# Performance work log

Measured on AMD Instinct MI355X. Metric: run time of the kernel, lower is better.

Reference implementation:

```python
import jax, jax.numpy as jnp
import numpy as np

B, T, C = 4, 2048, 1024
H, D = 16, 64           # num_heads, head_size
R = D // 2              # rotary_ndims = 32


def _make_rope(T, R):
    # RotaryEmbedding(dim=R): inv_freq over arange(0, R, 2)
    inv_freq = 1.0 / (10000.0 ** (np.arange(0, R, 2, dtype=np.float32) / R))
    t = np.arange(T, dtype=np.float32)
    freqs = np.einsum('i,j->ij', t, inv_freq)        # [T, R/2]
    emb = np.concatenate([freqs, freqs], axis=-1)    # [T, R]
    return jnp.asarray(np.stack([np.cos(emb), np.sin(emb)]), dtype=jnp.float32)  # [2, T, R]


def setup_inputs() -> dict:
    key = jax.random.key(0)
    ks = jax.random.split(key, 10)
    s = 1.0 / np.sqrt(C)
    inp = {
        'x': jax.random.normal(ks[0], (B, T, C), dtype=jnp.float32),
        'RoPE': _make_rope(T, R),
        'key_padding_mask': jax.random.randint(ks[1], (B, T), 0, 2, dtype=jnp.int32),
        'Wq': jax.random.normal(ks[2], (C, C), dtype=jnp.float32) * s,
        'bq': jnp.zeros((C,), dtype=jnp.float32),
        'Wk': jax.random.normal(ks[3], (C, C), dtype=jnp.float32) * s,
        'bk': jnp.zeros((C,), dtype=jnp.float32),
        'Wv': jax.random.normal(ks[4], (C, C), dtype=jnp.float32) * s,
        'bv': jnp.zeros((C,), dtype=jnp.float32),
        'Wo': jax.random.normal(ks[5], (C, C), dtype=jnp.float32) * s,
        'bo': jnp.zeros((C,), dtype=jnp.float32),
    }
    return inp


def _rotate_half(x):
    x1, x2 = x[..., : x.shape[-1] // 2], x[..., x.shape[-1] // 2:]
    return jnp.concatenate([-x2, x1], axis=-1)


def reference(x, RoPE, key_padding_mask, Wq, bq, Wk, bk, Wv, bv, Wo, bo):
    Bx, Tx, Cx = x.shape
    # projections -> [B, H, T, D]
    def proj(W, b):
        return (x @ W.T + b).reshape(Bx, Tx, H, D).transpose(0, 2, 1, 3)
    q, k, v = proj(Wq, bq), proj(Wk, bk), proj(Wv, bv)

    # partial rotary: first R dims rotated, rest passed through
    q_rot, q_pass = q[..., :R], q[..., R:]
    k_rot, k_pass = k[..., :R], k[..., R:]
    cos, sin = RoPE[0][:Tx], RoPE[1][:Tx]            # [T, R]
    q_rot = q_rot * cos + _rotate_half(q_rot) * sin
    k_rot = k_rot * cos + _rotate_half(k_rot) * sin
    q = jnp.concatenate([q_rot, q_pass], axis=-1)
    k = jnp.concatenate([k_rot, k_pass], axis=-1)

    att = jnp.einsum('bhqd,bhkd->bhqk', q, k) * (1.0 / np.sqrt(D))
    mask = key_padding_mask[:, None, None, :]        # [B,1,1,T]
    att = jnp.where(mask == 0, jnp.asarray(-1e30, att.dtype), att)
    att = jax.nn.softmax(att, axis=-1)
    out = jnp.einsum('bhqk,bhkd->bhqd', att, v)      # [B,H,T,D]
    out = out.transpose(0, 2, 1, 3).reshape(Bx, Tx, Cx)
    return out @ Wo.T + bo
```

## Files before the change

kernel.cpp:

```cpp
#include <hip/hip_runtime.h>
#include <stdint.h>


typedef __attribute__((ext_vector_type(8))) short bf16x8;
typedef __attribute__((ext_vector_type(4))) float f32x4;
typedef __attribute__((ext_vector_type(4))) short short4v;
typedef __attribute__((ext_vector_type(2))) uint32_t uint2v;

#define MFMA16(a, b, c) __builtin_amdgcn_mfma_f32_16x16x32_bf16((a), (b), (c), 0, 0, 0)

#if __has_builtin(__builtin_amdgcn_exp2f)
#define FEXP(x) __builtin_amdgcn_exp2f(x)
#define QSCALE 0.18033688011112042f
#else
#define FEXP(x) __expf(x)
#define QSCALE 0.125f
#endif

static __device__ __forceinline__ short f2bf(float f) {
  union { float fv; uint32_t u; } v; v.fv = f;
  uint32_t r = v.u + 0x7FFFu + ((v.u >> 16) & 1u);
  return (short)(r >> 16);
}

static __device__ __forceinline__ uint32_t pack_trunc(float a, float b) {
  union { float f; uint32_t u; } ua, ub;
  ua.f = a; ub.f = b;
#if __has_builtin(__builtin_amdgcn_perm)
  return __builtin_amdgcn_perm(ub.u, ua.u, 0x07060302u);
#else
  return (ub.u & 0xFFFF0000u) | (ua.u >> 16);
#endif
}

typedef __attribute__((address_space(1))) void as1_void;
typedef __attribute__((address_space(3))) void as3_void;
static __device__ __forceinline__ void gld_lds16(const void* g, void* l) {
  __builtin_amdgcn_global_load_lds((as1_void*)g, (as3_void*)l, 16, 0, 0);
}

__global__ __launch_bounds__(256) void cvt_kernel(
    const float* x, const float* wq, const float* wk, const float* wv,
    const float* wo,
    short* xb, short* wqb, short* wkb, short* wvb, short* wob) {
  int64_t g = (int64_t)blockIdx.x * 256 + threadIdx.x;
  const int64_t NX = 8388608 / 4, NW = 1048576 / 4;
  const float* src;
  short* dst;
  int64_t i;
  if (g < NX)               { src = x;  dst = xb;  i = g; }
  else if (g < NX + NW)     { src = wq; dst = wqb; i = g - NX; }
  else if (g < NX + 2 * NW) { src = wk; dst = wkb; i = g - NX - NW; }
  else if (g < NX + 3 * NW) { src = wv; dst = wvb; i = g - NX - 2 * NW; }
  else                      { src = wo; dst = wob; i = g - NX - 3 * NW; }
  float4 v = ((const float4*)src)[i];
  short4v o;
  o[0] = f2bf(v.x); o[1] = f2bf(v.y); o[2] = f2bf(v.z); o[3] = f2bf(v.w);
  *(short4v*)&dst[i * 4] = o;
}

__global__ __launch_bounds__(256, 2) void qkv3_gemm(
    const short* __restrict__ Xb,
    const short* __restrict__ Wq, const short* __restrict__ Wk,
    const short* __restrict__ Wv,
    const float* __restrict__ bq, const float* __restrict__ bk,
    const float* __restrict__ bv,
    const float* __restrict__ rope, const int* __restrict__ mask,
    short* __restrict__ Qh, short* __restrict__ Kh, short* __restrict__ Vt) {
  __shared__ __align__(16) short As[2][128 * 32];
  __shared__ __align__(16) short Bs[2][3][128 * 32];

  const int t = threadIdx.x;
  const int lane = t & 63;
  const int wave = t >> 6;
  const int c = lane & 15;
  const int quad = lane >> 4;
  const int m0 = blockIdx.x * 128;
  const int n0 = blockIdx.y * 128;

  f32x4 zero4 = {0.f, 0.f, 0.f, 0.f};
  f32x4 acc[3][4][4];
#pragma unroll
  for (int m = 0; m < 3; ++m)
#pragma unroll
    for (int i = 0; i < 4; ++i)
#pragma unroll
      for (int j = 0; j < 4; ++j) acc[m][i][j] = zero4;

  const int wm = wave & 1, wn = wave >> 1;

  const int srow = t >> 2;
  const int gc = ((t & 3) - (srow >> 2)) & 3;
  const short* gA = Xb + (size_t)(m0 + srow) * 1024 + gc * 8;
  const short* gW0 = Wq + (size_t)(n0 + srow) * 1024 + gc * 8;
  const short* gW1 = Wk + (size_t)(n0 + srow) * 1024 + gc * 8;
  const short* gW2 = Wv + (size_t)(n0 + srow) * 1024 + gc * 8;

#define QKV_STAGE(buf, k0)                                  \
  do {                                                      \
    gld_lds16(gA + (k0), &As[buf][t * 8]);                  \
    gld_lds16(gA + (k0) + 65536, &As[buf][t * 8 + 2048]);   \
    gld_lds16(gW0 + (k0), &Bs[buf][0][t * 8]);              \
    gld_lds16(gW0 + (k0) + 65536, &Bs[buf][0][t * 8 + 2048]); \
    gld_lds16(gW1 + (k0), &Bs[buf][1][t * 8]);              \
    gld_lds16(gW1 + (k0) + 65536, &Bs[buf][1][t * 8 + 2048]); \
    gld_lds16(gW2 + (k0), &Bs[buf][2][t * 8]);              \
    gld_lds16(gW2 + (k0) + 65536, &Bs[buf][2][t * 8 + 2048]); \
  } while (0)

  QKV_STAGE(0, 0);

  for (int ki = 0; ki < 32; ++ki) {
    __syncthreads();
    if (ki < 31) QKV_STAGE((ki + 1) & 1, (ki + 1) * 32);

    const short* as = &As[ki & 1][0];
    bf16x8 af[4];
#pragma unroll
    for (int i = 0; i < 4; ++i) {
      int mr = wm * 64 + i * 16 + c;
      af[i] = *(const bf16x8*)&as[mr * 32 + (((quad + (mr >> 2)) & 3) * 8)];
    }
#pragma unroll
    for (int m = 0; m < 3; ++m) {
      const short* bs = &Bs[ki & 1][m][0];
      bf16x8 bfr[4];
#pragma unroll
      for (int j = 0; j < 4; ++j) {
        int nr = wn * 64 + j * 16 + c;
        bfr[j] = *(const bf16x8*)&bs[nr * 32 + (((quad + (nr >> 2)) & 3) * 8)];
      }
#pragma unroll
      for (int i = 0; i < 4; ++i)
#pragma unroll
        for (int j = 0; j < 4; ++j)
          acc[m][i][j] = MFMA16(af[i], bfr[j], acc[m][i][j]);
    }
  }
#undef QKV_STAGE

  const int nb = n0 + wn * 64;
  const int hcol = nb >> 6;
  const int bidx = m0 >> 11;
  const int tbase = (m0 & 2047) + wm * 64 + quad * 4;
  const int* mrow = mask + bidx * 2048;

#pragma unroll
  for (int mat = 0; mat < 2; ++mat) {
    short* Og = (mat == 0) ? Qh : Kh;
    const float* bias = (mat == 0) ? bq : bk;
    float bj[4];
#pragma unroll
    for (int j = 0; j < 4; ++j) bj[j] = bias[nb + j * 16 + c];
    size_t hb = (size_t)(bidx * 16 + hcol) * 2048;
#pragma unroll
    for (int i = 0; i < 4; ++i) {
#pragma unroll
      for (int r = 0; r < 4; ++r) {
        int tp = tbase + i * 16 + r;
        float f = (mat == 0) ? QSCALE : (mrow[tp] ? 1.0f : 0.0f);
        float cosv = rope[tp * 32 + c];
        float sinv = rope[65536 + tp * 32 + c];
        float v0 = acc[mat][i][0][r] + bj[0];
        float v1 = acc[mat][i][1][r] + bj[1];
        float v2 = acc[mat][i][2][r] + bj[2];
        float v3 = acc[mat][i][3][r] + bj[3];
        size_t base = (hb + tp) * 64;
        Og[base + c]      = f2bf((v0 * cosv - v1 * sinv) * f);
        Og[base + 16 + c] = f2bf((v1 * cosv + v0 * sinv) * f);
        Og[base + 32 + c] = f2bf(v2 * f);
        Og[base + 48 + c] = f2bf(v3 * f);
      }
    }
  }
  {
    float bj[4];
#pragma unroll
    for (int j = 0; j < 4; ++j) bj[j] = bv[nb + j * 16 + c];
    size_t hb = (size_t)(bidx * 16 + hcol) * 64;
#pragma unroll
    for (int i = 0; i < 4; ++i) {
      int tp = tbase + i * 16;
      int4 mv = *(const int4*)&mrow[tp];
      float fr[4];
      fr[0] = mv.x ? 1.f : 0.f; fr[1] = mv.y ? 1.f : 0.f;
      fr[2] = mv.z ? 1.f : 0.f; fr[3] = mv.w ? 1.f : 0.f;
#pragma unroll
      for (int j = 0; j < 4; ++j) {
        short4v pv;
#pragma unroll
        for (int r = 0; r < 4; ++r)
          pv[r] = f2bf((acc[2][i][j][r] + bj[j]) * fr[r]);
        size_t base = (hb + j * 16 + c) * 2048 + tp;
        *(short4v*)&Vt[base] = pv;
      }
    }
  }
}

__global__ __launch_bounds__(256, 2) void attn_kernel(
    const short* __restrict__ Qh, const short* __restrict__ Kh,
    const short* __restrict__ Vt, const int* __restrict__ mask,
    short* __restrict__ Og) {
  __shared__ __align__(16) short Ks[2][64 * 64];
  __shared__ __align__(16) short Vs[2][64 * 64];
  __shared__ __align__(16) short Pl[4][32 * 64];
  __shared__ float nmw[4];

  const int t = threadIdx.x;
  const int lane = t & 63;
  const int wave = t >> 6;
  const int c = lane & 15;
  const int quad = lane >> 4;
  const int qt = blockIdx.x;
  const int bh = blockIdx.y;
  const int bidx = bh >> 4;
  const short* Qg = Qh + ((size_t)bh * 2048 + qt * 256) * 64;
  const short* Kg = Kh + (size_t)bh * 2048 * 64;
  const short* Vg = Vt + (size_t)bh * 64 * 2048;

  {
    const int4* mr = (const int4*)(mask + bidx * 2048);
    int4 a = mr[t * 2], b = mr[t * 2 + 1];
    int cnt = (a.x == 0) + (a.y == 0) + (a.z == 0) + (a.w == 0) +
              (b.x == 0) + (b.y == 0) + (b.z == 0) + (b.w == 0);
    cnt += __shfl_xor(cnt, 1);  cnt += __shfl_xor(cnt, 2);
    cnt += __shfl_xor(cnt, 4);  cnt += __shfl_xor(cnt, 8);
    cnt += __shfl_xor(cnt, 16); cnt += __shfl_xor(cnt, 32);
    if (lane == 0) nmw[wave] = (float)cnt;
  }

  bf16x8 qf[2][4];
#pragma unroll
  for (int ks = 0; ks < 2; ++ks)
#pragma unroll
    for (int it = 0; it < 4; ++it)
      qf[ks][it] =
          *(const bf16x8*)&Qg[(wave * 64 + it * 16 + c) * 64 + ks * 32 + quad * 8];

  const bf16x8 ones = {0x3F80, 0x3F80, 0x3F80, 0x3F80,
                       0x3F80, 0x3F80, 0x3F80, 0x3F80};

  f32x4 zero4 = {0.f, 0.f, 0.f, 0.f};
  f32x4 O[4][4];
#pragma unroll
  for (int dt = 0; dt < 4; ++dt)
#pragma unroll
    for (int it = 0; it < 4; ++it) O[dt][it] = zero4;
  f32x4 Ol[4] = {zero4, zero4, zero4, zero4};

  const int krow0 = t >> 3;
  const int klc = (t & 7) ^ (krow0 & 7);
  const short* gk0 = Kg + (size_t)krow0 * 64 + klc * 8;
  const short* gv0 = Vg + (size_t)krow0 * 2048 + klc * 8;
  short* Pw = &Pl[wave][0];

  gld_lds16(gk0, &Ks[0][t * 8]);
  gld_lds16(gk0 + 32 * 64, &Ks[0][t * 8 + 2048]);
  gld_lds16(gv0, &Vs[0][t * 8]);
  gld_lds16(gv0 + 32 * 2048, &Vs[0][t * 8 + 2048]);

  for (int ci = 0; ci < 32; ++ci) {
    __syncthreads();
    if (ci < 31) {
      int cn = (ci + 1) * 64;
      int nb = (ci + 1) & 1;
      gld_lds16(gk0 + (size_t)cn * 64, &Ks[nb][t * 8]);
      gld_lds16(gk0 + (size_t)(cn + 32) * 64, &Ks[nb][t * 8 + 2048]);
      gld_lds16(gv0 + cn, &Vs[nb][t * 8]);
      gld_lds16(gv0 + cn + 32 * 2048, &Vs[nb][t * 8 + 2048]);
    }
    const short* ksb = &Ks[ci & 1][0];
    const short* vsb = &Vs[ci & 1][0];

    bf16x8 ak[2][4], av[2][4];
#pragma unroll
    for (int ks = 0; ks < 2; ++ks)
#pragma unroll
      for (int jt = 0; jt < 4; ++jt) {
        ak[ks][jt] = *(const bf16x8*)&ksb[(jt * 16 + c) * 64 +
                                          (((4 * ks + quad) ^ (c & 7)) * 8)];
        av[ks][jt] = *(const bf16x8*)&vsb[(jt * 16 + c) * 64 +
                                          (((4 * ks + quad) ^ (c & 7)) * 8)];
      }

#pragma unroll
    for (int h = 0; h < 2; ++h) {
      f32x4 St[4][2];
#pragma unroll
      for (int jt = 0; jt < 4; ++jt) {
        St[jt][0] = MFMA16(ak[0][jt], qf[0][h * 2 + 0], zero4);
        St[jt][1] = MFMA16(ak[0][jt], qf[0][h * 2 + 1], zero4);
      }
#pragma unroll
      for (int jt = 0; jt < 4; ++jt) {
        St[jt][0] = MFMA16(ak[1][jt], qf[1][h * 2 + 0], St[jt][0]);
        St[jt][1] = MFMA16(ak[1][jt], qf[1][h * 2 + 1], St[jt][1]);
      }

#pragma unroll
      for (int itl = 0; itl < 2; ++itl) {
#pragma unroll
        for (int jt = 0; jt < 4; ++jt) {
          float p0 = FEXP(St[jt][itl][0]);
          float p1 = FEXP(St[jt][itl][1]);
          float p2 = FEXP(St[jt][itl][2]);
          float p3 = FEXP(St[jt][itl][3]);
          uint2v pk;
          pk[0] = pack_trunc(p0, p1);
          pk[1] = pack_trunc(p2, p3);
          *(uint2v*)&Pw[(itl * 16 + c) * 64 +
                        (((jt * 2 + (quad >> 1)) ^ (c & 7)) * 8) +
                        (quad & 1) * 4] = pk;
        }
      }
      asm volatile("s_waitcnt lgkmcnt(0)" ::: "memory");

#pragma unroll
      for (int ks = 0; ks < 2; ++ks) {
        bf16x8 bp0 =
            *(const bf16x8*)&Pw[c * 64 + (((ks * 4 + quad) ^ (c & 7)) * 8)];
        bf16x8 bp1 =
            *(const bf16x8*)&Pw[(16 + c) * 64 + (((ks * 4 + quad) ^ (c & 7)) * 8)];
        Ol[h * 2 + 0] = MFMA16(ones, bp0, Ol[h * 2 + 0]);
        Ol[h * 2 + 1] = MFMA16(ones, bp1, Ol[h * 2 + 1]);
#pragma unroll
        for (int dt = 0; dt < 4; ++dt) {
          O[dt][h * 2 + 0] = MFMA16(av[ks][dt], bp0, O[dt][h * 2 + 0]);
          O[dt][h * 2 + 1] = MFMA16(av[ks][dt], bp1, O[dt][h * 2 + 1]);
        }
      }
    }
  }

  float nm = nmw[0] + nmw[1] + nmw[2] + nmw[3];
#pragma unroll
  for (int it = 0; it < 4; ++it) {
    float inv = 1.0f / (Ol[it][0] - nm);
    int tq = qt * 256 + wave * 64 + it * 16 + c;
    size_t rb = ((size_t)bidx * 2048 + tq) * 1024 + (size_t)(bh & 15) * 64;
#pragma unroll
    for (int dt = 0; dt < 4; ++dt) {
      short4v ov;
#pragma unroll
      for (int r = 0; r < 4; ++r) ov[r] = f2bf(O[dt][it][r] * inv);
      *(short4v*)&Og[rb + dt * 16 + quad * 4] = ov;
    }
  }
}

__global__ __launch_bounds__(256) void out_gemm(
    const short* __restrict__ Ab, const short* __restrict__ Wob,
    const float* __restrict__ bo, float* __restrict__ out) {
  __shared__ __align__(16) short As[2][64 * 32];
  __shared__ __align__(16) short Bs[2][128 * 32];

  const int t = threadIdx.x;
  const int lane = t & 63;
  const int wave = t >> 6;
  const int c = lane & 15;
  const int quad = lane >> 4;
  const int m0 = blockIdx.x * 64;
  const int n0 = blockIdx.y * 128;

  f32x4 zero4 = {0.f, 0.f, 0.f, 0.f};
  f32x4 acc[4][2];
#pragma unroll
  for (int i = 0; i < 4; ++i) {
    acc[i][0] = zero4;
    acc[i][1] = zero4;
  }

  const int srow = t >> 2;
  const int gc = ((t & 3) - (srow >> 2)) & 3;
  const short* gA = Ab + (size_t)(m0 + srow) * 1024 + gc * 8;
  const short* gB = Wob + (size_t)(n0 + srow) * 1024 + gc * 8;

#define OUT_STAGE(buf, k0)                                   \
  do {                                                       \
    gld_lds16(gA + (k0), &As[buf][t * 8]);                   \
    gld_lds16(gB + (k0), &Bs[buf][t * 8]);                   \
    gld_lds16(gB + (k0) + 65536, &Bs[buf][t * 8 + 2048]);    \
  } while (0)

  OUT_STAGE(0, 0);

  for (int ki = 0; ki < 32; ++ki) {
    __syncthreads();
    if (ki < 31) OUT_STAGE((ki + 1) & 1, (ki + 1) * 32);

    const short* as = &As[ki & 1][0];
    const short* bs = &Bs[ki & 1][0];
    bf16x8 af[4], bfr[2];
#pragma unroll
    for (int i = 0; i < 4; ++i) {
      int mr = i * 16 + c;
      af[i] = *(const bf16x8*)&as[mr * 32 + (((quad + (mr >> 2)) & 3) * 8)];
    }
#pragma unroll
    for (int j = 0; j < 2; ++j) {
      int nr = wave * 32 + j * 16 + c;
      bfr[j] = *(const bf16x8*)&bs[nr * 32 + (((quad + (nr >> 2)) & 3) * 8)];
    }
#pragma unroll
    for (int i = 0; i < 4; ++i) {
      acc[i][0] = MFMA16(af[i], bfr[0], acc[i][0]);
      acc[i][1] = MFMA16(af[i], bfr[1], acc[i][1]);
    }
  }
#undef OUT_STAGE

  const int nb = n0 + wave * 32;
  float bj[2];
  bj[0] = bo[nb + c];
  bj[1] = bo[nb + 16 + c];
#pragma unroll
  for (int i = 0; i < 4; ++i) {
    int m = m0 + i * 16 + quad * 4;
#pragma unroll
    for (int r = 0; r < 4; ++r) {
      float* orow = out + (size_t)(m + r) * 1024 + nb;
      orow[c]      = acc[i][0][r] + bj[0];
      orow[16 + c] = acc[i][1][r] + bj[1];
    }
  }
}

extern "C" void kernel_launch(void* const* d_in, const int* in_sizes, int n_in,
                              void* d_out, int out_size, void* d_ws,
                              size_t ws_size, hipStream_t stream) {
  const float* x    = (const float*)d_in[0];
  const float* rope = (const float*)d_in[1];
  const int*   mask = (const int*)d_in[2];
  const float* Wq   = (const float*)d_in[3];
  const float* bq   = (const float*)d_in[4];
  const float* Wk   = (const float*)d_in[5];
  const float* bk   = (const float*)d_in[6];
  const float* Wv   = (const float*)d_in[7];
  const float* bv   = (const float*)d_in[8];
  const float* Wo   = (const float*)d_in[9];
  const float* bo   = (const float*)d_in[10];
  float* out = (float*)d_out;

  char* ws = (char*)d_ws;
  short* xb  = (short*)(ws);
  short* wqb = (short*)(ws + 16777216);
  short* wkb = (short*)(ws + 18874368);
  short* wvb = (short*)(ws + 20971520);
  short* wob = (short*)(ws + 23068672);
  short* Qh  = (short*)(ws + 25198592);
  short* Kh  = (short*)(ws + 41975808);
  short* Vt  = (short*)(ws + 58753024);
  short* att = xb;

  cvt_kernel<<<12288, 256, 0, stream>>>(x, Wq, Wk, Wv, Wo, xb, wqb, wkb, wvb,
                                        wob);
  qkv3_gemm<<<dim3(64, 8), 256, 0, stream>>>(xb, wqb, wkb, wvb, bq, bk, bv,
                                             rope, mask, Qh, Kh, Vt);
  attn_kernel<<<dim3(8, 64), 256, 0, stream>>>(Qh, Kh, Vt, mask, att);
  out_gemm<<<dim3(128, 8), 256, 0, stream>>>(att, wob, bo, out);
}
```

Measured before the change: 272.9 us.

## Halve attention query tile per block to raise occupancy and grid size

The attention kernel now processes 128 queries per block (32 per wave) instead of 256, doubling the grid to 1024 blocks and cutting per-wave accumulator registers and the P staging buffer in LDS. Launch bounds request 4 blocks per CU instead of 2. The grid is reordered so the head index is the fast dimension. Each wave now counts masked keys itself, removing the shared-memory reduction. The cost is that each block re-streams the full K/V sequence for half as many queries, doubling K/V load traffic and reducing MFMA reuse of each loaded K/V fragment.

Result: no change. 275.9 us (+1.1%).

```diff
diff --git a/kernel.cpp b/kernel.cpp
--- a/kernel.cpp
+++ b/kernel.cpp
@@ -198,56 +198,59 @@
   }
 }
 
-__global__ __launch_bounds__(256, 2) void attn_kernel(
+__global__ __launch_bounds__(256, 4) void attn_kernel(
     const short* __restrict__ Qh, const short* __restrict__ Kh,
     const short* __restrict__ Vt, const int* __restrict__ mask,
     short* __restrict__ Og) {
   __shared__ __align__(16) short Ks[2][64 * 64];
   __shared__ __align__(16) short Vs[2][64 * 64];
-  __shared__ __align__(16) short Pl[4][32 * 64];
-  __shared__ float nmw[4];
+  __shared__ __align__(16) short Pl[4][16 * 64];
 
   const int t = threadIdx.x;
   const int lane = t & 63;
   const int wave = t >> 6;
   const int c = lane & 15;
   const int quad = lane >> 4;
-  const int qt = blockIdx.x;
-  const int bh = blockIdx.y;
+  const int bh = blockIdx.x;
+  const int qt = blockIdx.y;
   const int bidx = bh >> 4;
-  const short* Qg = Qh + ((size_t)bh * 2048 + qt * 256) * 64;
+  const short* Qg = Qh + ((size_t)bh * 2048 + qt * 128) * 64;
   const short* Kg = Kh + (size_t)bh * 2048 * 64;
   const short* Vg = Vt + (size_t)bh * 64 * 2048;
 
+  float nm;
   {
     const int4* mr = (const int4*)(mask + bidx * 2048);
-    int4 a = mr[t * 2], b = mr[t * 2 + 1];
-    int cnt = (a.x == 0) + (a.y == 0) + (a.z == 0) + (a.w == 0) +
-              (b.x == 0) + (b.y == 0) + (b.z == 0) + (b.w == 0);
+    int cnt = 0;
+#pragma unroll
+    for (int k = 0; k < 8; ++k) {
+      int4 a = mr[k * 64 + lane];
+      cnt += (a.x == 0) + (a.y == 0) + (a.z == 0) + (a.w == 0);
+    }
     cnt += __shfl_xor(cnt, 1);  cnt += __shfl_xor(cnt, 2);
     cnt += __shfl_xor(cnt, 4);  cnt += __shfl_xor(cnt, 8);
     cnt += __shfl_xor(cnt, 16); cnt += __shfl_xor(cnt, 32);
-    if (lane == 0) nmw[wave] = (float)cnt;
-  }
-
-  bf16x8 qf[2][4];
+    nm = (float)cnt;
+  }
+
+  bf16x8 qf[2][2];
 #pragma unroll
   for (int ks = 0; ks < 2; ++ks)
 #pragma unroll
-    for (int it = 0; it < 4; ++it)
+    for (int it = 0; it < 2; ++it)
       qf[ks][it] =
-          *(const bf16x8*)&Qg[(wave * 64 + it * 16 + c) * 64 + ks * 32 + quad * 8];
+          *(const bf16x8*)&Qg[(wave * 32 + it * 16 + c) * 64 + ks * 32 + quad * 8];
 
   const bf16x8 ones = {0x3F80, 0x3F80, 0x3F80, 0x3F80,
                        0x3F80, 0x3F80, 0x3F80, 0x3F80};
 
   f32x4 zero4 = {0.f, 0.f, 0.f, 0.f};
-  f32x4 O[4][4];
+  f32x4 O[4][2];
 #pragma unroll
   for (int dt = 0; dt < 4; ++dt)
 #pragma unroll
-    for (int it = 0; it < 4; ++it) O[dt][it] = zero4;
-  f32x4 Ol[4] = {zero4, zero4, zero4, zero4};
+    for (int it = 0; it < 2; ++it) O[dt][it] = zero4;
+  f32x4 Ol[2] = {zero4, zero4};
 
   const int krow0 = t >> 3;
   const int klc = (t & 7) ^ (krow0 & 7);
@@ -285,59 +288,46 @@
       }
 
 #pragma unroll
-    for (int h = 0; h < 2; ++h) {
-      f32x4 St[4][2];
+    for (int it = 0; it < 2; ++it) {
+      f32x4 St[4];
+#pragma unroll
+      for (int jt = 0; jt < 4; ++jt)
+        St[jt] = MFMA16(ak[0][jt], qf[0][it], zero4);
+#pragma unroll
+      for (int jt = 0; jt < 4; ++jt)
+        St[jt] = MFMA16(ak[1][jt], qf[1][it], St[jt]);
+
 #pragma unroll
       for (int jt = 0; jt < 4; ++jt) {
-        St[jt][0] = MFMA16(ak[0][jt], qf[0][h * 2 + 0], zero4);
-        St[jt][1] = MFMA16(ak[0][jt], qf[0][h * 2 + 1], zero4);
-      }
-#pragma unroll
-      for (int jt = 0; jt < 4; ++jt) {
-        St[jt][0] = MFMA16(ak[1][jt], qf[1][h * 2 + 0], St[jt][0]);
-        St[jt][1] = MFMA16(ak[1][jt], qf[1][h * 2 + 1], St[jt][1]);
-      }
-
-#pragma unroll
-      for (int itl = 0; itl < 2; ++itl) {
-#pragma unroll
-        for (int jt = 0; jt < 4; ++jt) {
-          float p0 = FEXP(St[jt][itl][0]);
-          float p1 = FEXP(St[jt][itl][1]);
-          float p2 = FEXP(St[jt][itl][2]);
-          float p3 = FEXP(St[jt][itl][3]);
-          uint2v pk;
-          pk[0] = pack_trunc(p0, p1);
-          pk[1] = pack_trunc(p2, p3);
-          *(uint2v*)&Pw[(itl * 16 + c) * 64 +
-                        (((jt * 2 + (quad >> 1)) ^ (c & 7)) * 8) +
-                        (quad & 1) * 4] = pk;
-        }
+        float p0 = FEXP(St[jt][0]);
+        float p1 = FEXP(St[jt][1]);
+        float p2 = FEXP(St[jt][2]);
+        float p3 = FEXP(St[jt][3]);
+        uint2v pk;
+        pk[0] = pack_trunc(p0, p1);
+        pk[1] = pack_trunc(p2, p3);
+        *(uint2v*)&Pw[c * 64 +
+                      (((jt * 2 + (quad >> 1)) ^ (c & 7)) * 8) +
+                      (quad & 1) * 4] = pk;
       }
       asm volatile("s_waitcnt lgkmcnt(0)" ::: "memory");
 
 #pragma unroll
       for (int ks = 0; ks < 2; ++ks) {
-        bf16x8 bp0 =
+        bf16x8 bp =
             *(const bf16x8*)&Pw[c * 64 + (((ks * 4 + quad) ^ (c & 7)) * 8)];
-        bf16x8 bp1 =
-            *(const bf16x8*)&Pw[(16 + c) * 64 + (((ks * 4 + quad) ^ (c & 7)) * 8)];
-        Ol[h * 2 + 0] = MFMA16(ones, bp0, Ol[h * 2 + 0]);
-        Ol[h * 2 + 1] = MFMA16(ones, bp1, Ol[h * 2 + 1]);
-#pragma unroll
-        for (int dt = 0; dt < 4; ++dt) {
-          O[dt][h * 2 + 0] = MFMA16(av[ks][dt], bp0, O[dt][h * 2 + 0]);
-          O[dt][h * 2 + 1] = MFMA16(av[ks][dt], bp1, O[dt][h * 2 + 1]);
-        }
-      }
-    }
-  }
-
-  float nm = nmw[0] + nmw[1] + nmw[2] + nmw[3];
-#pragma unroll
-  for (int it = 0; it < 4; ++it) {
+        Ol[it] = MFMA16(ones, bp, Ol[it]);
+#pragma unroll
+        for (int dt = 0; dt < 4; ++dt)
+          O[dt][it] = MFMA16(av[ks][dt], bp, O[dt][it]);
+      }
+    }
+  }
+
+#pragma unroll
+  for (int it = 0; it < 2; ++it) {
     float inv = 1.0f / (Ol[it][0] - nm);
-    int tq = qt * 256 + wave * 64 + it * 16 + c;
+    int tq = qt * 128 + wave * 32 + it * 16 + c;
     size_t rb = ((size_t)bidx * 2048 + tq) * 1024 + (size_t)(bh & 15) * 64;
 #pragma unroll
     for (int dt = 0; dt < 4; ++dt) {
@@ -457,6 +447,6 @@
                                         wob);
   qkv3_gemm<<<dim3(64, 8), 256, 0, stream>>>(xb, wqb, wkb, wvb, bq, bk, bv,
                                              rope, mask, Qh, Kh, Vt);
-  attn_kernel<<<dim3(8, 64), 256, 0, stream>>>(Qh, Kh, Vt, mask, att);
+  attn_kernel<<<dim3(64, 16), 256, 0, stream>>>(Qh, Kh, Vt, mask, att);
   out_gemm<<<dim3(128, 8), 256, 0, stream>>>(att, wob, bo, out);
 }
```

## Double-buffer per-wave P tiles, relax LDS waits, reorder attention grid

Applied to the files above, without the earlier changes.

Each wave's P scratch in the attention kernel now has two halves, one per h-iteration. All exp/pack writes for both halves are issued before the PV MFMAs, and partial lgkmcnt waits replace the full drain so LDS writes overlap with compute. The masked-key count is now computed redundantly per wave, removing the shared nmw array and its implicit cross-wave dependency. The grid is transposed so blocks sharing a batch-head are launched adjacently, which may improve K/V cache reuse. LDS use grows by 16KB per block, which may reduce occupancy. The hand-counted lgkmcnt values are fragile and must match the compiler's instruction ordering.

Measured after the change: 266.4 us. 1.02x faster.

```diff
diff --git a/kernel.cpp b/kernel.cpp
--- a/kernel.cpp
+++ b/kernel.cpp
@@ -204,30 +204,33 @@
     short* __restrict__ Og) {
   __shared__ __align__(16) short Ks[2][64 * 64];
   __shared__ __align__(16) short Vs[2][64 * 64];
-  __shared__ __align__(16) short Pl[4][32 * 64];
-  __shared__ float nmw[4];
+  __shared__ __align__(16) short Pl[4][2][32 * 64];
 
   const int t = threadIdx.x;
   const int lane = t & 63;
   const int wave = t >> 6;
   const int c = lane & 15;
   const int quad = lane >> 4;
-  const int qt = blockIdx.x;
-  const int bh = blockIdx.y;
+  const int bh = blockIdx.x;
+  const int qt = blockIdx.y;
   const int bidx = bh >> 4;
   const short* Qg = Qh + ((size_t)bh * 2048 + qt * 256) * 64;
   const short* Kg = Kh + (size_t)bh * 2048 * 64;
   const short* Vg = Vt + (size_t)bh * 64 * 2048;
 
+  float nm;
   {
     const int4* mr = (const int4*)(mask + bidx * 2048);
-    int4 a = mr[t * 2], b = mr[t * 2 + 1];
-    int cnt = (a.x == 0) + (a.y == 0) + (a.z == 0) + (a.w == 0) +
-              (b.x == 0) + (b.y == 0) + (b.z == 0) + (b.w == 0);
+    int cnt = 0;
+#pragma unroll
+    for (int k = 0; k < 8; ++k) {
+      int4 a = mr[k * 64 + lane];
+      cnt += (a.x == 0) + (a.y == 0) + (a.z == 0) + (a.w == 0);
+    }
     cnt += __shfl_xor(cnt, 1);  cnt += __shfl_xor(cnt, 2);
     cnt += __shfl_xor(cnt, 4);  cnt += __shfl_xor(cnt, 8);
     cnt += __shfl_xor(cnt, 16); cnt += __shfl_xor(cnt, 32);
-    if (lane == 0) nmw[wave] = (float)cnt;
+    nm = (float)cnt;
   }
 
   bf16x8 qf[2][4];
@@ -253,7 +256,6 @@
   const int klc = (t & 7) ^ (krow0 & 7);
   const short* gk0 = Kg + (size_t)krow0 * 64 + klc * 8;
   const short* gv0 = Vg + (size_t)krow0 * 2048 + klc * 8;
-  short* Pw = &Pl[wave][0];
 
   gld_lds16(gk0, &Ks[0][t * 8]);
   gld_lds16(gk0 + 32 * 64, &Ks[0][t * 8 + 2048]);
@@ -297,7 +299,7 @@
         St[jt][0] = MFMA16(ak[1][jt], qf[1][h * 2 + 0], St[jt][0]);
         St[jt][1] = MFMA16(ak[1][jt], qf[1][h * 2 + 1], St[jt][1]);
       }
-
+      short* Ph = &Pl[wave][h][0];
 #pragma unroll
       for (int itl = 0; itl < 2; ++itl) {
 #pragma unroll
@@ -309,19 +311,25 @@
           uint2v pk;
           pk[0] = pack_trunc(p0, p1);
           pk[1] = pack_trunc(p2, p3);
-          *(uint2v*)&Pw[(itl * 16 + c) * 64 +
+          *(uint2v*)&Ph[(itl * 16 + c) * 64 +
                         (((jt * 2 + (quad >> 1)) ^ (c & 7)) * 8) +
                         (quad & 1) * 4] = pk;
         }
       }
-      asm volatile("s_waitcnt lgkmcnt(0)" ::: "memory");
-
+      asm volatile("" ::: "memory");
+    }
+
+    asm volatile("s_waitcnt lgkmcnt(8)" ::: "memory");
+
+#pragma unroll
+    for (int h = 0; h < 2; ++h) {
+      const short* Ph = &Pl[wave][h][0];
 #pragma unroll
       for (int ks = 0; ks < 2; ++ks) {
         bf16x8 bp0 =
-            *(const bf16x8*)&Pw[c * 64 + (((ks * 4 + quad) ^ (c & 7)) * 8)];
+            *(const bf16x8*)&Ph[c * 64 + (((ks * 4 + quad) ^ (c & 7)) * 8)];
         bf16x8 bp1 =
-            *(const bf16x8*)&Pw[(16 + c) * 64 + (((ks * 4 + quad) ^ (c & 7)) * 8)];
+            *(const bf16x8*)&Ph[(16 + c) * 64 + (((ks * 4 + quad) ^ (c & 7)) * 8)];
         Ol[h * 2 + 0] = MFMA16(ones, bp0, Ol[h * 2 + 0]);
         Ol[h * 2 + 1] = MFMA16(ones, bp1, Ol[h * 2 + 1]);
 #pragma unroll
@@ -330,10 +338,10 @@
           O[dt][h * 2 + 1] = MFMA16(av[ks][dt], bp1, O[dt][h * 2 + 1]);
         }
       }
-    }
-  }
-
-  float nm = nmw[0] + nmw[1] + nmw[2] + nmw[3];
+      if (h == 0) asm volatile("s_waitcnt lgkmcnt(4)" ::: "memory");
+    }
+  }
+
 #pragma unroll
   for (int it = 0; it < 4; ++it) {
     float inv = 1.0f / (Ol[it][0] - nm);
@@ -457,6 +465,6 @@
                                         wob);
   qkv3_gemm<<<dim3(64, 8), 256, 0, stream>>>(xb, wqb, wkb, wvb, bq, bk, bv,
                                              rope, mask, Qh, Kh, Vt);
-  attn_kernel<<<dim3(8, 64), 256, 0, stream>>>(Qh, Kh, Vt, mask, att);
+  attn_kernel<<<dim3(64, 8), 256, 0, stream>>>(Qh, Kh, Vt, mask, att);
   out_gemm<<<dim3(128, 8), 256, 0, stream>>>(att, wob, bo, out);
 }
```
